# Kernel tuning notes

Hardware: AMD Instinct MI355X
Metric: run time of the kernel (lower is better)

Reference implementation:

```python
import jax, jax.numpy as jnp
import numpy as np

N_RAYS = 65536
S_UNIFORM = 256          # 2 * n_samples coarse samples per ray
N_IMP = 128              # importance samples per ray
TRUNCATION = 2.0 / 512.0 * 4.0  # default in sdf2weights


def raw2weights_occupancy(raw):
    # raw2outputs_nerf_color with occupancy=True
    alpha = jax.nn.sigmoid(10.0 * raw)  # [N, S]
    trans = jnp.cumprod(
        jnp.concatenate([jnp.ones_like(alpha[:, :1]), 1.0 - alpha + 1e-10], axis=-1),
        axis=-1,
    )[:, :-1]
    return alpha, alpha * trans


def sample_pdf_det(bins, weights, n_samples):
    # bins: [N, M], weights: [N, M-1]; deterministic (det=True) inverse-CDF sampling
    w = weights + 1e-5
    pdf = w / jnp.sum(w, axis=-1, keepdims=True)
    cdf = jnp.cumsum(pdf, axis=-1)
    cdf = jnp.concatenate([jnp.zeros_like(cdf[..., :1]), cdf], axis=-1)  # [N, M]
    u = jnp.linspace(0.0, 1.0, n_samples, dtype=cdf.dtype)
    u = jnp.broadcast_to(u, cdf.shape[:-1] + (n_samples,))               # [N, n]
    inds = jax.vmap(lambda c, uu: jnp.searchsorted(c, uu, side='right'))(cdf, u)
    below = jnp.maximum(inds - 1, 0)
    above = jnp.minimum(inds, cdf.shape[-1] - 1)
    cdf_b = jnp.take_along_axis(cdf, below, axis=-1)
    cdf_a = jnp.take_along_axis(cdf, above, axis=-1)
    bins_b = jnp.take_along_axis(bins, below, axis=-1)
    bins_a = jnp.take_along_axis(bins, above, axis=-1)
    denom = cdf_a - cdf_b
    denom = jnp.where(denom < 1e-5, jnp.ones_like(denom), denom)
    t = (u - cdf_b) / denom
    return bins_b + t * (bins_a - bins_b)


def sdf2weights(sdf, z_vals, truncation=TRUNCATION, sc_factor=1.0):
    alpha = jax.nn.sigmoid(sdf / truncation) * jax.nn.sigmoid(-sdf / truncation)
    signs = sdf[:, 1:] * sdf[:, :-1]
    sign_mask = jnp.where(signs < 0.0, 1.0, 0.0)
    inds = jnp.argmax(sign_mask, axis=1)[:, None]              # first zero-crossing
    z_min = jnp.take_along_axis(z_vals, inds, axis=1)          # [N, 1]
    trunc_mask = jnp.where(z_vals < z_min + sc_factor * truncation, 1.0, 0.0)
    alpha = alpha * trunc_mask
    weights = alpha / (jnp.sum(alpha, axis=-1, keepdims=True) + 1e-8)
    return weights


def setup_inputs() -> dict:
    key = jax.random.key(0)
    k1, k2, k3, k4 = jax.random.split(key, 4)
    occ = jax.random.normal(k1, (N_RAYS, S_UNIFORM), dtype=jnp.float32)
    # monotonically increasing depths in [0.1, 4.1)
    z_vals_u = jnp.sort(
        jax.random.uniform(k2, (N_RAYS, S_UNIFORM), dtype=jnp.float32) * 4.0 + 0.1,
        axis=-1,
    )
    sdf = jax.random.normal(k3, (N_RAYS, N_IMP), dtype=jnp.float32) * 0.05
    rgbs = jax.random.uniform(k4, (N_RAYS, N_IMP, 3), dtype=jnp.float32)
    return {"occ": occ, "z_vals_u": z_vals_u, "sdf": sdf, "rgbs": rgbs}


def reference(occ, z_vals_u, sdf, rgbs):
    # 1) coarse occupancy compositing -> weights
    _, w_u = raw2weights_occupancy(occ)
    # 2) inverse-CDF importance sampling over midpoints (detached, as in gen_samples)
    z_mid = 0.5 * (z_vals_u[..., 1:] + z_vals_u[..., :-1])
    z_samples = jax.lax.stop_gradient(sample_pdf_det(z_mid, w_u[..., 1:-1], N_IMP))
    # 3) TSDF weights at importance samples
    weights = sdf2weights(sdf, z_samples)
    # 4) composite
    rgb_map = jnp.clip(jnp.sum(weights[..., None] * rgbs, axis=-2), 0.0, 1.0)  # [N,3]
    depth_map = jnp.sum(weights * z_samples, axis=-1)                          # [N]
    return jnp.concatenate([rgb_map, depth_map[:, None], weights], axis=-1)    # [N, 4+N_IMP]
```

## Files before the change

kernel.cpp:

```cpp
#include <hip/hip_runtime.h>
#include <limits.h>

#define S_U 256
#define N_IMP 128
#define OUT_STRIDE (4 + N_IMP)
#define TRUNC 0.015625f
#define WPB 4
#define INV127 (1.0f / 127.0f)

template<int CTRL, int RM, int BM>
__device__ __forceinline__ int dpp_i(int old_, int x) {
    return __builtin_amdgcn_update_dpp(old_, x, CTRL, RM, BM, false);
}
template<int CTRL, int RM, int BM>
__device__ __forceinline__ float dpp_f(float old_, float x) {
    return __int_as_float(__builtin_amdgcn_update_dpp(
        __float_as_int(old_), __float_as_int(x), CTRL, RM, BM, false));
}
__device__ __forceinline__ float readlane_f(float x, int l) {
    return __int_as_float(__builtin_amdgcn_readlane(__float_as_int(x), l));
}

__device__ __forceinline__ float wscan_add(float x) {
    x += dpp_f<0x111,0xf,0xf>(0.0f, x);
    x += dpp_f<0x112,0xf,0xf>(0.0f, x);
    x += dpp_f<0x114,0xf,0xf>(0.0f, x);
    x += dpp_f<0x118,0xf,0xf>(0.0f, x);
    x += dpp_f<0x142,0xa,0xf>(0.0f, x);
    x += dpp_f<0x143,0xc,0xf>(0.0f, x);
    return x;
}
__device__ __forceinline__ float wscan_mul(float x) {
    x *= dpp_f<0x111,0xf,0xf>(1.0f, x);
    x *= dpp_f<0x112,0xf,0xf>(1.0f, x);
    x *= dpp_f<0x114,0xf,0xf>(1.0f, x);
    x *= dpp_f<0x118,0xf,0xf>(1.0f, x);
    x *= dpp_f<0x142,0xa,0xf>(1.0f, x);
    x *= dpp_f<0x143,0xc,0xf>(1.0f, x);
    return x;
}
__device__ __forceinline__ int wscan_max(int x) {
    x = max(x, dpp_i<0x111,0xf,0xf>(0, x));
    x = max(x, dpp_i<0x112,0xf,0xf>(0, x));
    x = max(x, dpp_i<0x114,0xf,0xf>(0, x));
    x = max(x, dpp_i<0x118,0xf,0xf>(0, x));
    x = max(x, dpp_i<0x142,0xa,0xf>(0, x));
    x = max(x, dpp_i<0x143,0xc,0xf>(0, x));
    return x;
}
__device__ __forceinline__ int wred_min(int x) {
    x = min(x, dpp_i<0x111,0xf,0xf>(INT_MAX, x));
    x = min(x, dpp_i<0x112,0xf,0xf>(INT_MAX, x));
    x = min(x, dpp_i<0x114,0xf,0xf>(INT_MAX, x));
    x = min(x, dpp_i<0x118,0xf,0xf>(INT_MAX, x));
    x = min(x, dpp_i<0x142,0xa,0xf>(INT_MAX, x));
    x = min(x, dpp_i<0x143,0xc,0xf>(INT_MAX, x));
    return x;
}

__device__ __forceinline__ int jm_of(float c) {
    int jm = (int)ceilf(c * 127.0f);
    jm = min(max(jm, 0), 128);
    if (jm > 0 && (float)(jm - 1) * INV127 >= c) jm--;
    else if (jm < 128 && (float)jm * INV127 < c) jm++;
    return jm;
}

__global__ __launch_bounds__(256) void tsdf_render_kernel(
    const float* __restrict__ occ,
    const float* __restrict__ zvals,
    const float* __restrict__ sdf,
    const float* __restrict__ rgbs,
    float* __restrict__ out)
{
    const int lane = threadIdx.x & 63;
    const int wv   = threadIdx.x >> 6;
    const int ray  = blockIdx.x * WPB + wv;

    __shared__ __align__(16) float s_cdf [WPB][S_U];
    __shared__ __align__(16) float s_zmid[WPB][S_U];
    __shared__ __align__(16) int   s_bs  [WPB][N_IMP];

    const float4 o4  = ((const float4*)(occ   + (size_t)ray * S_U))[lane];
    const float4 z4  = ((const float4*)(zvals + (size_t)ray * S_U))[lane];
    const float2 sd2 = ((const float2*)(sdf   + (size_t)ray * N_IMP))[lane];
    const float2* rg = (const float2*)(rgbs + (size_t)ray * (N_IMP * 3)) + lane * 3;
    const float2 p0 = rg[0];
    const float2 p1 = rg[1];
    const float2 p2 = rg[2];

    float a0 = 1.0f / (1.0f + __expf(-10.0f * o4.x));
    float a1 = 1.0f / (1.0f + __expf(-10.0f * o4.y));
    float a2 = 1.0f / (1.0f + __expf(-10.0f * o4.z));
    float a3 = 1.0f / (1.0f + __expf(-10.0f * o4.w));
    float t0 = 1.0f - a0 + 1e-10f;
    float t1 = 1.0f - a1 + 1e-10f;
    float t2 = 1.0f - a2 + 1e-10f;
    float t3 = 1.0f - a3 + 1e-10f;

    float pp0 = t0, pp1 = pp0 * t1, pp2 = pp1 * t2, pp3 = pp2 * t3;
    float P = wscan_mul(pp3);
    float pbase = dpp_f<0x138,0xf,0xf>(1.0f, P);

    float w0 = a0 * pbase;
    float w1 = a1 * pbase * pp0;
    float w2 = a2 * pbase * pp1;
    float w3 = a3 * pbase * pp2;

    float v0 = (lane > 0)  ? w0 + 1e-5f : 0.0f;
    float v1 = w1 + 1e-5f;
    float v2 = w2 + 1e-5f;
    float v3 = (lane < 63) ? w3 + 1e-5f : 0.0f;
    float s0 = v0, s1 = s0 + v1, s2 = s1 + v2, s3 = s2 + v3;
    float S  = wscan_add(s3);
    float sbase = dpp_f<0x138,0xf,0xf>(0.0f, S);
    float total = readlane_f(S, 63);
    float invt = 1.0f / total;

    float4 cdf4;
    cdf4.x = (sbase + s0) * invt;
    cdf4.y = (sbase + s1) * invt;
    cdf4.z = (sbase + s2) * invt;
    cdf4.w = (sbase + s3) * invt;
    *((float4*)&s_cdf[wv][lane * 4]) = cdf4;

    float znext = dpp_f<0x130,0xf,0xf>(z4.x, z4.x);
    float4 zm4;
    zm4.x = 0.5f * (z4.x + z4.y);
    zm4.y = 0.5f * (z4.y + z4.z);
    zm4.z = 0.5f * (z4.z + z4.w);
    zm4.w = 0.5f * (z4.w + znext);
    *((float4*)&s_zmid[wv][lane * 4]) = zm4;

    *((int2*)&s_bs[wv][lane * 2]) = make_int2(0, 0);

    __builtin_amdgcn_wave_barrier();

    int jm0 = jm_of(cdf4.x);
    int jm1 = jm_of(cdf4.y);
    int jm2 = jm_of(cdf4.z);
    int jm3 = jm_of(cdf4.w);
    if (lane == 63) jm3 = 128;
    int jmn = dpp_i<0x130,0xf,0xf>(128, jm0);

    int ib = lane * 4;
    if (jm0 < jm1) s_bs[wv][jm0] = ib;
    if (jm1 < jm2) s_bs[wv][jm1] = ib + 1;
    if (jm2 < jm3) s_bs[wv][jm2] = ib + 2;
    if (jm3 < jmn) s_bs[wv][jm3] = ib + 3;

    __builtin_amdgcn_wave_barrier();

    int2 bse = *((const int2*)&s_bs[wv][lane * 2]);
    int H  = wscan_max(max(bse.x, bse.y));
    int Hp = dpp_i<0x138,0xf,0xf>(0, H);
    int b0 = max(Hp, bse.x);
    int b1 = H;

    const float* cdfp = s_cdf[wv];
    const float* zmp  = s_zmid[wv];
    float u0 = (float)(2 * lane)     * INV127;
    float u1 = (float)(2 * lane + 1) * INV127;

    float cb0 = cdfp[b0], ca0 = cdfp[b0 + 1];
    float zb0 = zmp[b0],  za0 = zmp[b0 + 1];
    float cb1 = cdfp[b1], ca1 = cdfp[b1 + 1];
    float zb1 = zmp[b1],  za1 = zmp[b1 + 1];

    float d0 = ca0 - cb0; d0 = (d0 < 1e-5f) ? 1.0f : d0;
    float d1 = ca1 - cb1; d1 = (d1 < 1e-5f) ? 1.0f : d1;
    float tt0 = (u0 - cb0) * __builtin_amdgcn_rcpf(d0);
    float tt1 = (u1 - cb1) * __builtin_amdgcn_rcpf(d1);
    float zs0 = zb0 + tt0 * (za0 - zb0);
    float zs1 = zb1 + tt1 * (za1 - zb1);

    float sn = dpp_f<0x130,0xf,0xf>(sd2.x, sd2.x);
    int c = INT_MAX;
    if (sd2.x * sd2.y < 0.0f)                  c = 2 * lane;
    else if (lane < 63 && sd2.y * sn < 0.0f)   c = 2 * lane + 1;
    c = wred_min(c);
    int cis = __builtin_amdgcn_readlane(c, 63);
    cis = (cis == INT_MAX) ? 0 : cis;
    float zca = readlane_f(zs0, cis >> 1);
    float zcb = readlane_f(zs1, cis >> 1);
    float z_min = (cis & 1) ? zcb : zca;

    float x0 = sd2.x * (1.0f / TRUNC);
    float x1 = sd2.y * (1.0f / TRUNC);
    float al0 = __builtin_amdgcn_rcpf(2.0f + __expf(x0) + __expf(-x0));
    float al1 = __builtin_amdgcn_rcpf(2.0f + __expf(x1) + __expf(-x1));
    float zlim = z_min + TRUNC;
    if (!(zs0 < zlim)) al0 = 0.0f;
    if (!(zs1 < zlim)) al1 = 0.0f;

    float At = wscan_add(al0 + al1);
    float asum = readlane_f(At, 63);
    float inv_s = __builtin_amdgcn_rcpf(asum + 1e-8f);
    float g0 = al0 * inv_s;
    float g1 = al1 * inv_s;

    float rr = wscan_add(g0 * p0.x + g1 * p1.y);
    float gg = wscan_add(g0 * p0.y + g1 * p2.x);
    float bb = wscan_add(g0 * p1.x + g1 * p2.y);
    float dd = wscan_add(g0 * zs0  + g1 * zs1);

    float* ob = out + (size_t)ray * OUT_STRIDE;
    ((float2*)(ob + 4))[lane] = make_float2(g0, g1);
    if (lane == 63) {
        ob[0] = fminf(fmaxf(rr, 0.0f), 1.0f);
        ob[1] = fminf(fmaxf(gg, 0.0f), 1.0f);
        ob[2] = fminf(fmaxf(bb, 0.0f), 1.0f);
        ob[3] = dd;
    }
}

extern "C" void kernel_launch(void* const* d_in, const int* in_sizes, int n_in,
                              void* d_out, int out_size, void* d_ws, size_t ws_size,
                              hipStream_t stream) {
    const float* occ  = (const float*)d_in[0];
    const float* z    = (const float*)d_in[1];
    const float* sdf  = (const float*)d_in[2];
    const float* rgbs = (const float*)d_in[3];
    float* out = (float*)d_out;
    const int n_rays = in_sizes[0] / S_U;
    hipLaunchKernelGGL(tsdf_render_kernel, dim3(n_rays / WPB), dim3(256), 0, stream,
                       occ, z, sdf, rgbs, out);
}
```

Baseline: 267.2 us.

## Use persistent grid-stride loop with software prefetch of next ray's occ/z

Replaces the one-ray-per-wave launch with a capped persistent grid (2048 blocks) where each wave loops over rays with grid stride. The next ray's occupancy and depth vectors are loaded before the current ray is computed, so their memory latency overlaps with compute. Launch bounds now request 8 blocks per CU, and wave barriers are added so the shared buffers can be reused safely across iterations. The risks are extra register pressure from the prefetched values and fewer waves in flight to hide the latency of the other loads (sdf, rgb).

```diff
diff --git a/kernel.cpp b/kernel.cpp
--- a/kernel.cpp
+++ b/kernel.cpp
@@ -7,6 +7,7 @@
 #define TRUNC 0.015625f
 #define WPB 4
 #define INV127 (1.0f / 127.0f)
+#define MAX_BLOCKS 2048
 
 template<int CTRL, int RM, int BM>
 __device__ __forceinline__ int dpp_i(int old_, int x) {
@@ -66,151 +67,168 @@
     return jm;
 }
 
-__global__ __launch_bounds__(256) void tsdf_render_kernel(
+__global__ __launch_bounds__(256, 8) void tsdf_render_kernel(
     const float* __restrict__ occ,
     const float* __restrict__ zvals,
     const float* __restrict__ sdf,
     const float* __restrict__ rgbs,
-    float* __restrict__ out)
+    float* __restrict__ out,
+    int n_rays)
 {
     const int lane = threadIdx.x & 63;
     const int wv   = threadIdx.x >> 6;
-    const int ray  = blockIdx.x * WPB + wv;
+    const int rstride = gridDim.x * WPB;
+    int ray = blockIdx.x * WPB + wv;
 
     __shared__ __align__(16) float s_cdf [WPB][S_U];
     __shared__ __align__(16) float s_zmid[WPB][S_U];
     __shared__ __align__(16) int   s_bs  [WPB][N_IMP];
 
-    const float4 o4  = ((const float4*)(occ   + (size_t)ray * S_U))[lane];
-    const float4 z4  = ((const float4*)(zvals + (size_t)ray * S_U))[lane];
-    const float2 sd2 = ((const float2*)(sdf   + (size_t)ray * N_IMP))[lane];
-    const float2* rg = (const float2*)(rgbs + (size_t)ray * (N_IMP * 3)) + lane * 3;
-    const float2 p0 = rg[0];
-    const float2 p1 = rg[1];
-    const float2 p2 = rg[2];
-
-    float a0 = 1.0f / (1.0f + __expf(-10.0f * o4.x));
-    float a1 = 1.0f / (1.0f + __expf(-10.0f * o4.y));
-    float a2 = 1.0f / (1.0f + __expf(-10.0f * o4.z));
-    float a3 = 1.0f / (1.0f + __expf(-10.0f * o4.w));
-    float t0 = 1.0f - a0 + 1e-10f;
-    float t1 = 1.0f - a1 + 1e-10f;
-    float t2 = 1.0f - a2 + 1e-10f;
-    float t3 = 1.0f - a3 + 1e-10f;
-
-    float pp0 = t0, pp1 = pp0 * t1, pp2 = pp1 * t2, pp3 = pp2 * t3;
-    float P = wscan_mul(pp3);
-    float pbase = dpp_f<0x138,0xf,0xf>(1.0f, P);
-
-    float w0 = a0 * pbase;
-    float w1 = a1 * pbase * pp0;
-    float w2 = a2 * pbase * pp1;
-    float w3 = a3 * pbase * pp2;
-
-    float v0 = (lane > 0)  ? w0 + 1e-5f : 0.0f;
-    float v1 = w1 + 1e-5f;
-    float v2 = w2 + 1e-5f;
-    float v3 = (lane < 63) ? w3 + 1e-5f : 0.0f;
-    float s0 = v0, s1 = s0 + v1, s2 = s1 + v2, s3 = s2 + v3;
-    float S  = wscan_add(s3);
-    float sbase = dpp_f<0x138,0xf,0xf>(0.0f, S);
-    float total = readlane_f(S, 63);
-    float invt = 1.0f / total;
-
-    float4 cdf4;
-    cdf4.x = (sbase + s0) * invt;
-    cdf4.y = (sbase + s1) * invt;
-    cdf4.z = (sbase + s2) * invt;
-    cdf4.w = (sbase + s3) * invt;
-    *((float4*)&s_cdf[wv][lane * 4]) = cdf4;
-
-    float znext = dpp_f<0x130,0xf,0xf>(z4.x, z4.x);
-    float4 zm4;
-    zm4.x = 0.5f * (z4.x + z4.y);
-    zm4.y = 0.5f * (z4.y + z4.z);
-    zm4.z = 0.5f * (z4.z + z4.w);
-    zm4.w = 0.5f * (z4.w + znext);
-    *((float4*)&s_zmid[wv][lane * 4]) = zm4;
-
-    *((int2*)&s_bs[wv][lane * 2]) = make_int2(0, 0);
-
-    __builtin_amdgcn_wave_barrier();
-
-    int jm0 = jm_of(cdf4.x);
-    int jm1 = jm_of(cdf4.y);
-    int jm2 = jm_of(cdf4.z);
-    int jm3 = jm_of(cdf4.w);
-    if (lane == 63) jm3 = 128;
-    int jmn = dpp_i<0x130,0xf,0xf>(128, jm0);
-
-    int ib = lane * 4;
-    if (jm0 < jm1) s_bs[wv][jm0] = ib;
-    if (jm1 < jm2) s_bs[wv][jm1] = ib + 1;
-    if (jm2 < jm3) s_bs[wv][jm2] = ib + 2;
-    if (jm3 < jmn) s_bs[wv][jm3] = ib + 3;
-
-    __builtin_amdgcn_wave_barrier();
-
-    int2 bse = *((const int2*)&s_bs[wv][lane * 2]);
-    int H  = wscan_max(max(bse.x, bse.y));
-    int Hp = dpp_i<0x138,0xf,0xf>(0, H);
-    int b0 = max(Hp, bse.x);
-    int b1 = H;
-
-    const float* cdfp = s_cdf[wv];
-    const float* zmp  = s_zmid[wv];
-    float u0 = (float)(2 * lane)     * INV127;
-    float u1 = (float)(2 * lane + 1) * INV127;
-
-    float cb0 = cdfp[b0], ca0 = cdfp[b0 + 1];
-    float zb0 = zmp[b0],  za0 = zmp[b0 + 1];
-    float cb1 = cdfp[b1], ca1 = cdfp[b1 + 1];
-    float zb1 = zmp[b1],  za1 = zmp[b1 + 1];
-
-    float d0 = ca0 - cb0; d0 = (d0 < 1e-5f) ? 1.0f : d0;
-    float d1 = ca1 - cb1; d1 = (d1 < 1e-5f) ? 1.0f : d1;
-    float tt0 = (u0 - cb0) * __builtin_amdgcn_rcpf(d0);
-    float tt1 = (u1 - cb1) * __builtin_amdgcn_rcpf(d1);
-    float zs0 = zb0 + tt0 * (za0 - zb0);
-    float zs1 = zb1 + tt1 * (za1 - zb1);
-
-    float sn = dpp_f<0x130,0xf,0xf>(sd2.x, sd2.x);
-    int c = INT_MAX;
-    if (sd2.x * sd2.y < 0.0f)                  c = 2 * lane;
-    else if (lane < 63 && sd2.y * sn < 0.0f)   c = 2 * lane + 1;
-    c = wred_min(c);
-    int cis = __builtin_amdgcn_readlane(c, 63);
-    cis = (cis == INT_MAX) ? 0 : cis;
-    float zca = readlane_f(zs0, cis >> 1);
-    float zcb = readlane_f(zs1, cis >> 1);
-    float z_min = (cis & 1) ? zcb : zca;
-
-    float x0 = sd2.x * (1.0f / TRUNC);
-    float x1 = sd2.y * (1.0f / TRUNC);
-    float al0 = __builtin_amdgcn_rcpf(2.0f + __expf(x0) + __expf(-x0));
-    float al1 = __builtin_amdgcn_rcpf(2.0f + __expf(x1) + __expf(-x1));
-    float zlim = z_min + TRUNC;
-    if (!(zs0 < zlim)) al0 = 0.0f;
-    if (!(zs1 < zlim)) al1 = 0.0f;
-
-    float At = wscan_add(al0 + al1);
-    float asum = readlane_f(At, 63);
-    float inv_s = __builtin_amdgcn_rcpf(asum + 1e-8f);
-    float g0 = al0 * inv_s;
-    float g1 = al1 * inv_s;
-
-    float rr = wscan_add(g0 * p0.x + g1 * p1.y);
-    float gg = wscan_add(g0 * p0.y + g1 * p2.x);
-    float bb = wscan_add(g0 * p1.x + g1 * p2.y);
-    float dd = wscan_add(g0 * zs0  + g1 * zs1);
-
-    float* ob = out + (size_t)ray * OUT_STRIDE;
-    ((float2*)(ob + 4))[lane] = make_float2(g0, g1);
-    if (lane == 63) {
-        ob[0] = fminf(fmaxf(rr, 0.0f), 1.0f);
-        ob[1] = fminf(fmaxf(gg, 0.0f), 1.0f);
-        ob[2] = fminf(fmaxf(bb, 0.0f), 1.0f);
-        ob[3] = dd;
+    if (ray >= n_rays) return;
+
+    float4 o4 = ((const float4*)(occ   + (size_t)ray * S_U))[lane];
+    float4 z4 = ((const float4*)(zvals + (size_t)ray * S_U))[lane];
+
+    for (;;) {
+        const float2 sd2 = ((const float2*)(sdf + (size_t)ray * N_IMP))[lane];
+        const float2* rg = (const float2*)(rgbs + (size_t)ray * (N_IMP * 3)) + lane * 3;
+        const float2 p0 = rg[0];
+        const float2 p1 = rg[1];
+        const float2 p2 = rg[2];
+
+        const int nray = ray + rstride;
+        const bool more = nray < n_rays;
+        float4 o4n, z4n;
+        if (more) {
+            o4n = ((const float4*)(occ   + (size_t)nray * S_U))[lane];
+            z4n = ((const float4*)(zvals + (size_t)nray * S_U))[lane];
+        }
+
+        float a0 = 1.0f / (1.0f + __expf(-10.0f * o4.x));
+        float a1 = 1.0f / (1.0f + __expf(-10.0f * o4.y));
+        float a2 = 1.0f / (1.0f + __expf(-10.0f * o4.z));
+        float a3 = 1.0f / (1.0f + __expf(-10.0f * o4.w));
+        float t0 = 1.0f - a0 + 1e-10f;
+        float t1 = 1.0f - a1 + 1e-10f;
+        float t2 = 1.0f - a2 + 1e-10f;
+        float t3 = 1.0f - a3 + 1e-10f;
+
+        float pp0 = t0, pp1 = pp0 * t1, pp2 = pp1 * t2, pp3 = pp2 * t3;
+        float P = wscan_mul(pp3);
+        float pbase = dpp_f<0x138,0xf,0xf>(1.0f, P);
+
+        float w0 = a0 * pbase;
+        float w1 = a1 * pbase * pp0;
+        float w2 = a2 * pbase * pp1;
+        float w3 = a3 * pbase * pp2;
+
+        float v0 = (lane > 0)  ? w0 + 1e-5f : 0.0f;
+        float v1 = w1 + 1e-5f;
+        float v2 = w2 + 1e-5f;
+        float v3 = (lane < 63) ? w3 + 1e-5f : 0.0f;
+        float s0 = v0, s1 = s0 + v1, s2 = s1 + v2, s3 = s2 + v3;
+        float S  = wscan_add(s3);
+        float sbase = dpp_f<0x138,0xf,0xf>(0.0f, S);
+        float total = readlane_f(S, 63);
+        float invt = 1.0f / total;
+
+        float4 cdf4;
+        cdf4.x = (sbase + s0) * invt;
+        cdf4.y = (sbase + s1) * invt;
+        cdf4.z = (sbase + s2) * invt;
+        cdf4.w = (sbase + s3) * invt;
+
+        float znext = dpp_f<0x130,0xf,0xf>(z4.x, z4.x);
+        float4 zm4;
+        zm4.x = 0.5f * (z4.x + z4.y);
+        zm4.y = 0.5f * (z4.y + z4.z);
+        zm4.z = 0.5f * (z4.z + z4.w);
+        zm4.w = 0.5f * (z4.w + znext);
+
+        __builtin_amdgcn_wave_barrier();
+        *((float4*)&s_cdf [wv][lane * 4]) = cdf4;
+        *((float4*)&s_zmid[wv][lane * 4]) = zm4;
+        *((int2*)&s_bs[wv][lane * 2]) = make_int2(0, 0);
+        __builtin_amdgcn_wave_barrier();
+
+        int jm0 = jm_of(cdf4.x);
+        int jm1 = jm_of(cdf4.y);
+        int jm2 = jm_of(cdf4.z);
+        int jm3 = jm_of(cdf4.w);
+        if (lane == 63) jm3 = 128;
+        int jmn = dpp_i<0x130,0xf,0xf>(128, jm0);
+
+        int ib = lane * 4;
+        if (jm0 < jm1) s_bs[wv][jm0] = ib;
+        if (jm1 < jm2) s_bs[wv][jm1] = ib + 1;
+        if (jm2 < jm3) s_bs[wv][jm2] = ib + 2;
+        if (jm3 < jmn) s_bs[wv][jm3] = ib + 3;
+        __builtin_amdgcn_wave_barrier();
+
+        int2 bse = *((const int2*)&s_bs[wv][lane * 2]);
+        int H  = wscan_max(max(bse.x, bse.y));
+        int Hp = dpp_i<0x138,0xf,0xf>(0, H);
+        int b0 = max(Hp, bse.x);
+        int b1 = H;
+
+        const float* cdfp = s_cdf[wv];
+        const float* zmp  = s_zmid[wv];
+        float u0 = (float)(2 * lane)     * INV127;
+        float u1 = (float)(2 * lane + 1) * INV127;
+
+        float cb0 = cdfp[b0], ca0 = cdfp[b0 + 1];
+        float zb0 = zmp[b0],  za0 = zmp[b0 + 1];
+        float cb1 = cdfp[b1], ca1 = cdfp[b1 + 1];
+        float zb1 = zmp[b1],  za1 = zmp[b1 + 1];
+
+        float d0 = ca0 - cb0; d0 = (d0 < 1e-5f) ? 1.0f : d0;
+        float d1 = ca1 - cb1; d1 = (d1 < 1e-5f) ? 1.0f : d1;
+        float tt0 = (u0 - cb0) * __builtin_amdgcn_rcpf(d0);
+        float tt1 = (u1 - cb1) * __builtin_amdgcn_rcpf(d1);
+        float zs0 = zb0 + tt0 * (za0 - zb0);
+        float zs1 = zb1 + tt1 * (za1 - zb1);
+
+        float sn = dpp_f<0x130,0xf,0xf>(sd2.x, sd2.x);
+        int c = INT_MAX;
+        if (sd2.x * sd2.y < 0.0f)                  c = 2 * lane;
+        else if (lane < 63 && sd2.y * sn < 0.0f)   c = 2 * lane + 1;
+        c = wred_min(c);
+        int cis = __builtin_amdgcn_readlane(c, 63);
+        cis = (cis == INT_MAX) ? 0 : cis;
+        float zca = readlane_f(zs0, cis >> 1);
+        float zcb = readlane_f(zs1, cis >> 1);
+        float z_min = (cis & 1) ? zcb : zca;
+
+        float x0 = sd2.x * (1.0f / TRUNC);
+        float x1 = sd2.y * (1.0f / TRUNC);
+        float al0 = __builtin_amdgcn_rcpf(2.0f + __expf(x0) + __expf(-x0));
+        float al1 = __builtin_amdgcn_rcpf(2.0f + __expf(x1) + __expf(-x1));
+        float zlim = z_min + TRUNC;
+        if (!(zs0 < zlim)) al0 = 0.0f;
+        if (!(zs1 < zlim)) al1 = 0.0f;
+
+        float At = wscan_add(al0 + al1);
+        float asum = readlane_f(At, 63);
+        float inv_s = __builtin_amdgcn_rcpf(asum + 1e-8f);
+        float g0 = al0 * inv_s;
+        float g1 = al1 * inv_s;
+
+        float rr = wscan_add(g0 * p0.x + g1 * p1.y);
+        float gg = wscan_add(g0 * p0.y + g1 * p2.x);
+        float bb = wscan_add(g0 * p1.x + g1 * p2.y);
+        float dd = wscan_add(g0 * zs0  + g1 * zs1);
+
+        float* ob = out + (size_t)ray * OUT_STRIDE;
+        ((float2*)(ob + 4))[lane] = make_float2(g0, g1);
+        if (lane == 63) {
+            ob[0] = fminf(fmaxf(rr, 0.0f), 1.0f);
+            ob[1] = fminf(fmaxf(gg, 0.0f), 1.0f);
+            ob[2] = fminf(fmaxf(bb, 0.0f), 1.0f);
+            ob[3] = dd;
+        }
+
+        if (!more) break;
+        o4 = o4n; z4 = z4n; ray = nray;
     }
 }
 
@@ -223,6 +241,8 @@
     const float* rgbs = (const float*)d_in[3];
     float* out = (float*)d_out;
     const int n_rays = in_sizes[0] / S_U;
-    hipLaunchKernelGGL(tsdf_render_kernel, dim3(n_rays / WPB), dim3(256), 0, stream,
-                       occ, z, sdf, rgbs, out);
-}
+    int nblk = (n_rays + WPB - 1) / WPB;
+    if (nblk > MAX_BLOCKS) nblk = MAX_BLOCKS;
+    hipLaunchKernelGGL(tsdf_render_kernel, dim3(nblk), dim3(256), 0, stream,
+                       occ, z, sdf, rgbs, out, n_rays);
+}
```

Result: slower. 274.2 us (+2.6%).

## Process two rays per wavefront to interleave independent scan chains

Applied to the files above, without the earlier changes.

Each wavefront now handles two rays instead of one, so the grid shrinks by half and shared memory per block doubles. The two rays' DPP scans, LDS lookups and reductions are interleaved to expose instruction-level parallelism and hide the latency of the serial scan chains, and more loads are in flight per wave. In exchange it raises register and LDS use per block, which may lower occupancy.

```diff
diff --git a/kernel.cpp b/kernel.cpp
--- a/kernel.cpp
+++ b/kernel.cpp
@@ -6,6 +6,7 @@
 #define OUT_STRIDE (4 + N_IMP)
 #define TRUNC 0.015625f
 #define WPB 4
+#define RPB (WPB * 2)
 #define INV127 (1.0f / 127.0f)
 
 template<int CTRL, int RM, int BM>
@@ -64,6 +65,48 @@
     if (jm > 0 && (float)(jm - 1) * INV127 >= c) jm--;
     else if (jm < 128 && (float)jm * INV127 < c) jm++;
     return jm;
+}
+
+__device__ __forceinline__ void coarse_cdf(const float4 o4, const float4 z4,
+                                           int lane, float4& cdf4, float4& zm4) {
+    float a0 = 1.0f / (1.0f + __expf(-10.0f * o4.x));
+    float a1 = 1.0f / (1.0f + __expf(-10.0f * o4.y));
+    float a2 = 1.0f / (1.0f + __expf(-10.0f * o4.z));
+    float a3 = 1.0f / (1.0f + __expf(-10.0f * o4.w));
+    float t0 = 1.0f - a0 + 1e-10f;
+    float t1 = 1.0f - a1 + 1e-10f;
+    float t2 = 1.0f - a2 + 1e-10f;
+    float t3 = 1.0f - a3 + 1e-10f;
+
+    float pp0 = t0, pp1 = pp0 * t1, pp2 = pp1 * t2, pp3 = pp2 * t3;
+    float P = wscan_mul(pp3);
+    float pbase = dpp_f<0x138,0xf,0xf>(1.0f, P);
+
+    float w0 = a0 * pbase;
+    float w1 = a1 * pbase * pp0;
+    float w2 = a2 * pbase * pp1;
+    float w3 = a3 * pbase * pp2;
+
+    float v0 = (lane > 0)  ? w0 + 1e-5f : 0.0f;
+    float v1 = w1 + 1e-5f;
+    float v2 = w2 + 1e-5f;
+    float v3 = (lane < 63) ? w3 + 1e-5f : 0.0f;
+    float s0 = v0, s1 = s0 + v1, s2 = s1 + v2, s3 = s2 + v3;
+    float S  = wscan_add(s3);
+    float sbase = dpp_f<0x138,0xf,0xf>(0.0f, S);
+    float total = readlane_f(S, 63);
+    float invt = 1.0f / total;
+
+    cdf4.x = (sbase + s0) * invt;
+    cdf4.y = (sbase + s1) * invt;
+    cdf4.z = (sbase + s2) * invt;
+    cdf4.w = (sbase + s3) * invt;
+
+    float znext = dpp_f<0x130,0xf,0xf>(z4.x, z4.x);
+    zm4.x = 0.5f * (z4.x + z4.y);
+    zm4.y = 0.5f * (z4.y + z4.z);
+    zm4.z = 0.5f * (z4.z + z4.w);
+    zm4.w = 0.5f * (z4.w + znext);
 }
 
 __global__ __launch_bounds__(256) void tsdf_render_kernel(
@@ -75,142 +118,163 @@
 {
     const int lane = threadIdx.x & 63;
     const int wv   = threadIdx.x >> 6;
-    const int ray  = blockIdx.x * WPB + wv;
-
-    __shared__ __align__(16) float s_cdf [WPB][S_U];
-    __shared__ __align__(16) float s_zmid[WPB][S_U];
-    __shared__ __align__(16) int   s_bs  [WPB][N_IMP];
-
-    const float4 o4  = ((const float4*)(occ   + (size_t)ray * S_U))[lane];
-    const float4 z4  = ((const float4*)(zvals + (size_t)ray * S_U))[lane];
-    const float2 sd2 = ((const float2*)(sdf   + (size_t)ray * N_IMP))[lane];
-    const float2* rg = (const float2*)(rgbs + (size_t)ray * (N_IMP * 3)) + lane * 3;
-    const float2 p0 = rg[0];
-    const float2 p1 = rg[1];
-    const float2 p2 = rg[2];
-
-    float a0 = 1.0f / (1.0f + __expf(-10.0f * o4.x));
-    float a1 = 1.0f / (1.0f + __expf(-10.0f * o4.y));
-    float a2 = 1.0f / (1.0f + __expf(-10.0f * o4.z));
-    float a3 = 1.0f / (1.0f + __expf(-10.0f * o4.w));
-    float t0 = 1.0f - a0 + 1e-10f;
-    float t1 = 1.0f - a1 + 1e-10f;
-    float t2 = 1.0f - a2 + 1e-10f;
-    float t3 = 1.0f - a3 + 1e-10f;
-
-    float pp0 = t0, pp1 = pp0 * t1, pp2 = pp1 * t2, pp3 = pp2 * t3;
-    float P = wscan_mul(pp3);
-    float pbase = dpp_f<0x138,0xf,0xf>(1.0f, P);
-
-    float w0 = a0 * pbase;
-    float w1 = a1 * pbase * pp0;
-    float w2 = a2 * pbase * pp1;
-    float w3 = a3 * pbase * pp2;
-
-    float v0 = (lane > 0)  ? w0 + 1e-5f : 0.0f;
-    float v1 = w1 + 1e-5f;
-    float v2 = w2 + 1e-5f;
-    float v3 = (lane < 63) ? w3 + 1e-5f : 0.0f;
-    float s0 = v0, s1 = s0 + v1, s2 = s1 + v2, s3 = s2 + v3;
-    float S  = wscan_add(s3);
-    float sbase = dpp_f<0x138,0xf,0xf>(0.0f, S);
-    float total = readlane_f(S, 63);
-    float invt = 1.0f / total;
-
-    float4 cdf4;
-    cdf4.x = (sbase + s0) * invt;
-    cdf4.y = (sbase + s1) * invt;
-    cdf4.z = (sbase + s2) * invt;
-    cdf4.w = (sbase + s3) * invt;
-    *((float4*)&s_cdf[wv][lane * 4]) = cdf4;
-
-    float znext = dpp_f<0x130,0xf,0xf>(z4.x, z4.x);
-    float4 zm4;
-    zm4.x = 0.5f * (z4.x + z4.y);
-    zm4.y = 0.5f * (z4.y + z4.z);
-    zm4.z = 0.5f * (z4.z + z4.w);
-    zm4.w = 0.5f * (z4.w + znext);
-    *((float4*)&s_zmid[wv][lane * 4]) = zm4;
-
-    *((int2*)&s_bs[wv][lane * 2]) = make_int2(0, 0);
-
+    const int rayA = blockIdx.x * RPB + wv * 2;
+    const int rayB = rayA + 1;
+    const int rA = wv * 2, rB = rA + 1;
+
+    __shared__ __align__(16) float s_cdf [RPB][S_U];
+    __shared__ __align__(16) float s_zmid[RPB][S_U];
+    __shared__ __align__(16) int   s_bs  [RPB][N_IMP];
+
+    const float4 o4A = ((const float4*)(occ   + (size_t)rayA * S_U))[lane];
+    const float4 z4A = ((const float4*)(zvals + (size_t)rayA * S_U))[lane];
+    const float4 o4B = ((const float4*)(occ   + (size_t)rayB * S_U))[lane];
+    const float4 z4B = ((const float4*)(zvals + (size_t)rayB * S_U))[lane];
+
+    float4 cdf4A, zm4A, cdf4B, zm4B;
+    coarse_cdf(o4A, z4A, lane, cdf4A, zm4A);
+    coarse_cdf(o4B, z4B, lane, cdf4B, zm4B);
+
+    const float2 sd2A = ((const float2*)(sdf + (size_t)rayA * N_IMP))[lane];
+    const float2 sd2B = ((const float2*)(sdf + (size_t)rayB * N_IMP))[lane];
+    const float2* rgA = (const float2*)(rgbs + (size_t)rayA * (N_IMP * 3)) + lane * 3;
+    const float2* rgB = (const float2*)(rgbs + (size_t)rayB * (N_IMP * 3)) + lane * 3;
+    const float2 p0A = rgA[0], p1A = rgA[1], p2A = rgA[2];
+    const float2 p0B = rgB[0], p1B = rgB[1], p2B = rgB[2];
+
+    *((float4*)&s_cdf [rA][lane * 4]) = cdf4A;
+    *((float4*)&s_zmid[rA][lane * 4]) = zm4A;
+    *((float4*)&s_cdf [rB][lane * 4]) = cdf4B;
+    *((float4*)&s_zmid[rB][lane * 4]) = zm4B;
+    *((int2*)&s_bs[rA][lane * 2]) = make_int2(0, 0);
+    *((int2*)&s_bs[rB][lane * 2]) = make_int2(0, 0);
     __builtin_amdgcn_wave_barrier();
 
-    int jm0 = jm_of(cdf4.x);
-    int jm1 = jm_of(cdf4.y);
-    int jm2 = jm_of(cdf4.z);
-    int jm3 = jm_of(cdf4.w);
-    if (lane == 63) jm3 = 128;
-    int jmn = dpp_i<0x130,0xf,0xf>(128, jm0);
-
-    int ib = lane * 4;
-    if (jm0 < jm1) s_bs[wv][jm0] = ib;
-    if (jm1 < jm2) s_bs[wv][jm1] = ib + 1;
-    if (jm2 < jm3) s_bs[wv][jm2] = ib + 2;
-    if (jm3 < jmn) s_bs[wv][jm3] = ib + 3;
-
+    {
+        int jm0 = jm_of(cdf4A.x), jm1 = jm_of(cdf4A.y);
+        int jm2 = jm_of(cdf4A.z), jm3 = jm_of(cdf4A.w);
+        if (lane == 63) jm3 = 128;
+        int jmn = dpp_i<0x130,0xf,0xf>(128, jm0);
+        int ib = lane * 4;
+        if (jm0 < jm1) s_bs[rA][jm0] = ib;
+        if (jm1 < jm2) s_bs[rA][jm1] = ib + 1;
+        if (jm2 < jm3) s_bs[rA][jm2] = ib + 2;
+        if (jm3 < jmn) s_bs[rA][jm3] = ib + 3;
+    }
+    {
+        int jm0 = jm_of(cdf4B.x), jm1 = jm_of(cdf4B.y);
+        int jm2 = jm_of(cdf4B.z), jm3 = jm_of(cdf4B.w);
+        if (lane == 63) jm3 = 128;
+        int jmn = dpp_i<0x130,0xf,0xf>(128, jm0);
+        int ib = lane * 4;
+        if (jm0 < jm1) s_bs[rB][jm0] = ib;
+        if (jm1 < jm2) s_bs[rB][jm1] = ib + 1;
+        if (jm2 < jm3) s_bs[rB][jm2] = ib + 2;
+        if (jm3 < jmn) s_bs[rB][jm3] = ib + 3;
+    }
     __builtin_amdgcn_wave_barrier();
 
-    int2 bse = *((const int2*)&s_bs[wv][lane * 2]);
-    int H  = wscan_max(max(bse.x, bse.y));
-    int Hp = dpp_i<0x138,0xf,0xf>(0, H);
-    int b0 = max(Hp, bse.x);
-    int b1 = H;
-
-    const float* cdfp = s_cdf[wv];
-    const float* zmp  = s_zmid[wv];
+    int2 bseA = *((const int2*)&s_bs[rA][lane * 2]);
+    int2 bseB = *((const int2*)&s_bs[rB][lane * 2]);
+    int HA  = wscan_max(max(bseA.x, bseA.y));
+    int HB  = wscan_max(max(bseB.x, bseB.y));
+    int HpA = dpp_i<0x138,0xf,0xf>(0, HA);
+    int HpB = dpp_i<0x138,0xf,0xf>(0, HB);
+    int b0A = max(HpA, bseA.x), b1A = HA;
+    int b0B = max(HpB, bseB.x), b1B = HB;
+
     float u0 = (float)(2 * lane)     * INV127;
     float u1 = (float)(2 * lane + 1) * INV127;
 
-    float cb0 = cdfp[b0], ca0 = cdfp[b0 + 1];
-    float zb0 = zmp[b0],  za0 = zmp[b0 + 1];
-    float cb1 = cdfp[b1], ca1 = cdfp[b1 + 1];
-    float zb1 = zmp[b1],  za1 = zmp[b1 + 1];
-
-    float d0 = ca0 - cb0; d0 = (d0 < 1e-5f) ? 1.0f : d0;
-    float d1 = ca1 - cb1; d1 = (d1 < 1e-5f) ? 1.0f : d1;
-    float tt0 = (u0 - cb0) * __builtin_amdgcn_rcpf(d0);
-    float tt1 = (u1 - cb1) * __builtin_amdgcn_rcpf(d1);
-    float zs0 = zb0 + tt0 * (za0 - zb0);
-    float zs1 = zb1 + tt1 * (za1 - zb1);
-
-    float sn = dpp_f<0x130,0xf,0xf>(sd2.x, sd2.x);
-    int c = INT_MAX;
-    if (sd2.x * sd2.y < 0.0f)                  c = 2 * lane;
-    else if (lane < 63 && sd2.y * sn < 0.0f)   c = 2 * lane + 1;
-    c = wred_min(c);
-    int cis = __builtin_amdgcn_readlane(c, 63);
-    cis = (cis == INT_MAX) ? 0 : cis;
-    float zca = readlane_f(zs0, cis >> 1);
-    float zcb = readlane_f(zs1, cis >> 1);
-    float z_min = (cis & 1) ? zcb : zca;
-
-    float x0 = sd2.x * (1.0f / TRUNC);
-    float x1 = sd2.y * (1.0f / TRUNC);
-    float al0 = __builtin_amdgcn_rcpf(2.0f + __expf(x0) + __expf(-x0));
-    float al1 = __builtin_amdgcn_rcpf(2.0f + __expf(x1) + __expf(-x1));
-    float zlim = z_min + TRUNC;
-    if (!(zs0 < zlim)) al0 = 0.0f;
-    if (!(zs1 < zlim)) al1 = 0.0f;
-
-    float At = wscan_add(al0 + al1);
-    float asum = readlane_f(At, 63);
-    float inv_s = __builtin_amdgcn_rcpf(asum + 1e-8f);
-    float g0 = al0 * inv_s;
-    float g1 = al1 * inv_s;
-
-    float rr = wscan_add(g0 * p0.x + g1 * p1.y);
-    float gg = wscan_add(g0 * p0.y + g1 * p2.x);
-    float bb = wscan_add(g0 * p1.x + g1 * p2.y);
-    float dd = wscan_add(g0 * zs0  + g1 * zs1);
-
-    float* ob = out + (size_t)ray * OUT_STRIDE;
-    ((float2*)(ob + 4))[lane] = make_float2(g0, g1);
+    const float* cdfpA = s_cdf[rA];
+    const float* zmpA  = s_zmid[rA];
+    float cb0A = cdfpA[b0A], ca0A = cdfpA[b0A + 1];
+    float zb0A = zmpA[b0A],  za0A = zmpA[b0A + 1];
+    float cb1A = cdfpA[b1A], ca1A = cdfpA[b1A + 1];
+    float zb1A = zmpA[b1A],  za1A = zmpA[b1A + 1];
+
+    const float* cdfpB = s_cdf[rB];
+    const float* zmpB  = s_zmid[rB];
+    float cb0B = cdfpB[b0B], ca0B = cdfpB[b0B + 1];
+    float zb0B = zmpB[b0B],  za0B = zmpB[b0B + 1];
+    float cb1B = cdfpB[b1B], ca1B = cdfpB[b1B + 1];
+    float zb1B = zmpB[b1B],  za1B = zmpB[b1B + 1];
+
+    float d0A = ca0A - cb0A; d0A = (d0A < 1e-5f) ? 1.0f : d0A;
+    float d1A = ca1A - cb1A; d1A = (d1A < 1e-5f) ? 1.0f : d1A;
+    float d0B = ca0B - cb0B; d0B = (d0B < 1e-5f) ? 1.0f : d0B;
+    float d1B = ca1B - cb1B; d1B = (d1B < 1e-5f) ? 1.0f : d1B;
+    float tt0A = (u0 - cb0A) * __builtin_amdgcn_rcpf(d0A);
+    float tt1A = (u1 - cb1A) * __builtin_amdgcn_rcpf(d1A);
+    float tt0B = (u0 - cb0B) * __builtin_amdgcn_rcpf(d0B);
+    float tt1B = (u1 - cb1B) * __builtin_amdgcn_rcpf(d1B);
+    float zs0A = zb0A + tt0A * (za0A - zb0A);
+    float zs1A = zb1A + tt1A * (za1A - zb1A);
+    float zs0B = zb0B + tt0B * (za0B - zb0B);
+    float zs1B = zb1B + tt1B * (za1B - zb1B);
+
+    float snA = dpp_f<0x130,0xf,0xf>(sd2A.x, sd2A.x);
+    float snB = dpp_f<0x130,0xf,0xf>(sd2B.x, sd2B.x);
+    int cA = INT_MAX, cB = INT_MAX;
+    if (sd2A.x * sd2A.y < 0.0f)                 cA = 2 * lane;
+    else if (lane < 63 && sd2A.y * snA < 0.0f)  cA = 2 * lane + 1;
+    if (sd2B.x * sd2B.y < 0.0f)                 cB = 2 * lane;
+    else if (lane < 63 && sd2B.y * snB < 0.0f)  cB = 2 * lane + 1;
+    cA = wred_min(cA);
+    cB = wred_min(cB);
+    int ciA = __builtin_amdgcn_readlane(cA, 63);
+    int ciB = __builtin_amdgcn_readlane(cB, 63);
+    ciA = (ciA == INT_MAX) ? 0 : ciA;
+    ciB = (ciB == INT_MAX) ? 0 : ciB;
+    float zcaA = readlane_f(zs0A, ciA >> 1);
+    float zcbA = readlane_f(zs1A, ciA >> 1);
+    float zcaB = readlane_f(zs0B, ciB >> 1);
+    float zcbB = readlane_f(zs1B, ciB >> 1);
+    float z_minA = (ciA & 1) ? zcbA : zcaA;
+    float z_minB = (ciB & 1) ? zcbB : zcaB;
+
+    float x0A = sd2A.x * (1.0f / TRUNC), x1A = sd2A.y * (1.0f / TRUNC);
+    float x0B = sd2B.x * (1.0f / TRUNC), x1B = sd2B.y * (1.0f / TRUNC);
+    float al0A = __builtin_amdgcn_rcpf(2.0f + __expf(x0A) + __expf(-x0A));
+    float al1A = __builtin_amdgcn_rcpf(2.0f + __expf(x1A) + __expf(-x1A));
+    float al0B = __builtin_amdgcn_rcpf(2.0f + __expf(x0B) + __expf(-x0B));
+    float al1B = __builtin_amdgcn_rcpf(2.0f + __expf(x1B) + __expf(-x1B));
+    float zlimA = z_minA + TRUNC;
+    float zlimB = z_minB + TRUNC;
+    if (!(zs0A < zlimA)) al0A = 0.0f;
+    if (!(zs1A < zlimA)) al1A = 0.0f;
+    if (!(zs0B < zlimB)) al0B = 0.0f;
+    if (!(zs1B < zlimB)) al1B = 0.0f;
+
+    float AtA = wscan_add(al0A + al1A);
+    float AtB = wscan_add(al0B + al1B);
+    float inv_sA = __builtin_amdgcn_rcpf(readlane_f(AtA, 63) + 1e-8f);
+    float inv_sB = __builtin_amdgcn_rcpf(readlane_f(AtB, 63) + 1e-8f);
+    float g0A = al0A * inv_sA, g1A = al1A * inv_sA;
+    float g0B = al0B * inv_sB, g1B = al1B * inv_sB;
+
+    float rrA = wscan_add(g0A * p0A.x + g1A * p1A.y);
+    float ggA = wscan_add(g0A * p0A.y + g1A * p2A.x);
+    float bbA = wscan_add(g0A * p1A.x + g1A * p2A.y);
+    float ddA = wscan_add(g0A * zs0A  + g1A * zs1A);
+    float rrB = wscan_add(g0B * p0B.x + g1B * p1B.y);
+    float ggB = wscan_add(g0B * p0B.y + g1B * p2B.x);
+    float bbB = wscan_add(g0B * p1B.x + g1B * p2B.y);
+    float ddB = wscan_add(g0B * zs0B  + g1B * zs1B);
+
+    float* obA = out + (size_t)rayA * OUT_STRIDE;
+    float* obB = out + (size_t)rayB * OUT_STRIDE;
+    ((float2*)(obA + 4))[lane] = make_float2(g0A, g1A);
+    ((float2*)(obB + 4))[lane] = make_float2(g0B, g1B);
     if (lane == 63) {
-        ob[0] = fminf(fmaxf(rr, 0.0f), 1.0f);
-        ob[1] = fminf(fmaxf(gg, 0.0f), 1.0f);
-        ob[2] = fminf(fmaxf(bb, 0.0f), 1.0f);
-        ob[3] = dd;
+        obA[0] = fminf(fmaxf(rrA, 0.0f), 1.0f);
+        obA[1] = fminf(fmaxf(ggA, 0.0f), 1.0f);
+        obA[2] = fminf(fmaxf(bbA, 0.0f), 1.0f);
+        obA[3] = ddA;
+        obB[0] = fminf(fmaxf(rrB, 0.0f), 1.0f);
+        obB[1] = fminf(fmaxf(ggB, 0.0f), 1.0f);
+        obB[2] = fminf(fmaxf(bbB, 0.0f), 1.0f);
+        obB[3] = ddB;
     }
 }
 
@@ -223,6 +287,6 @@
     const float* rgbs = (const float*)d_in[3];
     float* out = (float*)d_out;
     const int n_rays = in_sizes[0] / S_U;
-    hipLaunchKernelGGL(tsdf_render_kernel, dim3(n_rays / WPB), dim3(256), 0, stream,
+    hipLaunchKernelGGL(tsdf_render_kernel, dim3(n_rays / RPB), dim3(256), 0, stream,
                        occ, z, sdf, rgbs, out);
 }
```

Result: no change. 268.9 us (+0.7%).
